# Performance work log

Hardware: AMD Instinct MI355X
Metric: run time of the kernel (lower is better)

## Reference

```python
import jax, jax.numpy as jnp
import numpy as np

D_MODEL = 1024
N_HEAD = 16
D_K = D_MODEL // N_HEAD
NEG = -1000000000.0


def setup_inputs() -> dict:
    key = jax.random.key(0)
    ks = jax.random.split(key, 12)
    B, S = 4, 2048
    scale = 1.0 / np.sqrt(D_MODEL)
    inp = {
        "q": jax.random.normal(ks[0], (B, S, D_MODEL), jnp.float32),
        "k": jax.random.normal(ks[1], (B, S, D_MODEL), jnp.float32),
        "v": jax.random.normal(ks[2], (B, S, D_MODEL), jnp.float32),
        "mask": jnp.ones((1, 1, S, S), jnp.int32),
        "w_Q": jax.random.normal(ks[3], (D_MODEL, D_MODEL), jnp.float32) * scale,
        "b_Q": jnp.zeros((D_MODEL,), jnp.float32),
        "w_K": jax.random.normal(ks[4], (D_MODEL, D_MODEL), jnp.float32) * scale,
        "b_K": jnp.zeros((D_MODEL,), jnp.float32),
        "w_V": jax.random.normal(ks[5], (D_MODEL, D_MODEL), jnp.float32) * scale,
        "b_V": jnp.zeros((D_MODEL,), jnp.float32),
        "w_O": jax.random.normal(ks[6], (D_MODEL, D_MODEL), jnp.float32) * scale,
        "b_O": jnp.zeros((D_MODEL,), jnp.float32),
    }
    return inp


def reference(q, k, v, mask, w_Q, b_Q, w_K, b_K, w_V, b_V, w_O, b_O):
    B, S, _ = q.shape
    # linear projections (torch Linear: x @ W^T + b)
    qp = q @ w_Q.T + b_Q
    kp = k @ w_K.T + b_K
    vp = v @ w_V.T + b_V
    # [B,S,D] -> [B,H,S,d_k]
    qh = qp.reshape(B, S, N_HEAD, D_K).transpose(0, 2, 1, 3)
    kh = kp.reshape(B, S, N_HEAD, D_K).transpose(0, 2, 1, 3)
    vh = vp.reshape(B, S, N_HEAD, D_K).transpose(0, 2, 1, 3)
    # scores [B,H,S,S]
    scores = jnp.einsum("bhqd,bhkd->bhqk", qh, kh) / jnp.sqrt(jnp.float32(D_K))
    scores = jnp.where(mask == 0, jnp.float32(NEG), scores)
    attn = jax.nn.softmax(scores, axis=-1)  # dropout p=0.0 -> identity
    ctx = jnp.einsum("bhqk,bhkd->bhqd", attn, vh)
    ctx = ctx.transpose(0, 2, 1, 3).reshape(B, S, D_MODEL)
    return ctx @ w_O.T + b_O
```

## Files before the change

kernel.cpp:

```cpp
#include <hip/hip_runtime.h>
#include <hip/hip_bf16.h>
#include <cmath>

#define D_MODEL 1024
#define N_HEAD 16
#define D_K 64

typedef __attribute__((ext_vector_type(8))) short short8;
typedef __attribute__((ext_vector_type(4))) float f32x4;
typedef __attribute__((ext_vector_type(16))) float f32x16;

#define GL_LDS16(gp, lp)                                                                   \
  __builtin_amdgcn_global_load_lds((const __attribute__((address_space(1))) unsigned int*)(gp), \
                                   (__attribute__((address_space(3))) unsigned int*)(lp), 16, 0, 0)

#if __has_builtin(__builtin_amdgcn_exp2f)
#define EXP2(x) __builtin_amdgcn_exp2f(x)
#else
#define EXP2(x) exp2f(x)
#endif

__device__ __forceinline__ unsigned short f2bu(float x) {
  __hip_bfloat16 h = __float2bfloat16(x);
  return *reinterpret_cast<unsigned short*>(&h);
}

__device__ __forceinline__ unsigned int cvtpk(float lo, float hi) {
  unsigned int r;
  asm("v_cvt_pk_bf16_f32 %0, %1, %2" : "=v"(r) : "v"(lo), "v"(hi));
  return r;
}

__device__ __forceinline__ float max3f(float a, float b, float c) {
  return fmaxf(fmaxf(a, b), c);
}

__device__ __forceinline__ void plswap(unsigned int& a, unsigned int& b) {
#if __has_builtin(__builtin_amdgcn_permlane32_swap)
  auto r = __builtin_amdgcn_permlane32_swap((int)a, (int)b, false, false);
  a = (unsigned int)r[0];
  b = (unsigned int)r[1];
#else
  unsigned int ax = (unsigned int)__shfl_xor((int)a, 32);
  unsigned int bx = (unsigned int)__shfl_xor((int)b, 32);
  bool hi = (threadIdx.x & 32) != 0;
  unsigned int na = hi ? bx : a;
  unsigned int nb = hi ? b : ax;
  a = na; b = nb;
#endif
}

__global__ __launch_bounds__(256) void f2b3_kernel(const float* __restrict__ a, const float* __restrict__ b,
                                                   const float* __restrict__ c,
                                                   unsigned short* __restrict__ oa, unsigned short* __restrict__ ob,
                                                   unsigned short* __restrict__ oc, int n) {
  const float* src = (blockIdx.y == 0) ? a : (blockIdx.y == 1) ? b : c;
  unsigned short* dst = (blockIdx.y == 0) ? oa : (blockIdx.y == 1) ? ob : oc;
  int i = (blockIdx.x * 256 + threadIdx.x) * 4;
  if (i >= n) return;
  float4 v = *reinterpret_cast<const float4*>(src + i);
  ushort4 o;
  o.x = f2bu(v.x); o.y = f2bu(v.y); o.z = f2bu(v.z); o.w = f2bu(v.w);
  *reinterpret_cast<ushort4*>(dst + i) = o;
}

__global__ __launch_bounds__(256) void f2b4_kernel(const float* __restrict__ a, const float* __restrict__ b,
                                                   const float* __restrict__ c, const float* __restrict__ d,
                                                   unsigned short* __restrict__ oa, unsigned short* __restrict__ ob,
                                                   unsigned short* __restrict__ oc, unsigned short* __restrict__ od,
                                                   int n) {
  const float* src = (blockIdx.y == 0) ? a : (blockIdx.y == 1) ? b : (blockIdx.y == 2) ? c : d;
  unsigned short* dst = (blockIdx.y == 0) ? oa : (blockIdx.y == 1) ? ob : (blockIdx.y == 2) ? oc : od;
  int i = (blockIdx.x * 256 + threadIdx.x) * 4;
  if (i >= n) return;
  float4 v = *reinterpret_cast<const float4*>(src + i);
  ushort4 o;
  o.x = f2bu(v.x); o.y = f2bu(v.y); o.z = f2bu(v.z); o.w = f2bu(v.w);
  *reinterpret_cast<ushort4*>(dst + i) = o;
}

template <int OUTF32>
__global__ __launch_bounds__(256) void gemm_bt_kernel(
    const unsigned short* __restrict__ A0, const unsigned short* __restrict__ A1,
    const unsigned short* __restrict__ A2,
    const unsigned short* __restrict__ W0, const unsigned short* __restrict__ W1,
    const unsigned short* __restrict__ W2,
    const float* __restrict__ b0, const float* __restrict__ b1, const float* __restrict__ b2,
    void* __restrict__ Cout, int Msub, int N, int K,
    float s0, float s1, float s2) {
  __shared__ __align__(16) unsigned short lA[3][128 * 32];
  __shared__ __align__(16) unsigned short lB[3][128 * 32];

  const int tid = threadIdx.x;
  const int lane = tid & 63;
  const int w = tid >> 6;
  const int wm = w >> 1, wn = w & 1;
  const int lr = lane & 15, lg = lane >> 4;
  const int wavebase = tid & ~63;

  int m0g, n0;
  {
    const int nbx = gridDim.x;
    const int nb = nbx * gridDim.y;
    int lin = blockIdx.y * nbx + blockIdx.x;
    int wid = lin;
    if ((nb & 7) == 0) wid = (lin & 7) * (nb >> 3) + (lin >> 3);
    n0 = (wid % nbx) * 128;
    m0g = (wid / nbx) * 128;
  }
  const int mtile = m0g >> 7;
  const int which = mtile / (Msub >> 7);
  const int m0 = m0g - which * Msub;
  const unsigned short* A  = (which == 0) ? A0 : (which == 1) ? A1 : A2;
  const unsigned short* Bw = (which == 0) ? W0 : (which == 1) ? W1 : W2;
  const float* bias = (which == 0) ? b0 : (which == 1) ? b1 : b2;
  const float oscale = (which == 0) ? s0 : (which == 1) ? s1 : s2;

  f32x4 acc[4][4] = {};

  const int swz = (lg ^ (lr & 3) ^ ((lr >> 2) & 3)) << 4;
  int avA[4], avB[4];
#pragma unroll
  for (int m = 0; m < 4; ++m) {
    avA[m] = (wm * 64 + m * 16 + lr) * 64 + swz;
    avB[m] = (wn * 64 + m * 16 + lr) * 64 + swz;
  }

  auto stage = [&](int buf, int k0) {
#pragma unroll
    for (int j = 0; j < 2; ++j) {
      int c = j * 256 + tid;
      int row = c >> 2, cc = c & 3;
      int gc = (cc ^ (row & 3) ^ ((row >> 2) & 3)) * 8;
      GL_LDS16(A + (size_t)(m0 + row) * K + k0 + gc,
               (char*)&lA[buf][0] + (j * 256 + wavebase) * 16);
    }
#pragma unroll
    for (int j = 0; j < 2; ++j) {
      int c = j * 256 + tid;
      int row = c >> 2, cc = c & 3;
      int gc = (cc ^ (row & 3) ^ ((row >> 2) & 3)) * 8;
      GL_LDS16(Bw + (size_t)(n0 + row) * K + k0 + gc,
               (char*)&lB[buf][0] + (j * 256 + wavebase) * 16);
    }
  };

  const int nk = K / 32;
  stage(0, 0);
  stage(1, 32);
  stage(2, 64);

  int buf = 0;
  for (int t = 0; t < nk; ++t) {
    if (t < nk - 2)       asm volatile("s_waitcnt vmcnt(8)" ::: "memory");
    else if (t == nk - 2) asm volatile("s_waitcnt vmcnt(4)" ::: "memory");
    else                  asm volatile("s_waitcnt vmcnt(0)" ::: "memory");
    __builtin_amdgcn_s_barrier();
    __builtin_amdgcn_sched_barrier(0);

    const char* pA = (const char*)&lA[buf][0];
    const char* pB = (const char*)&lB[buf][0];
    short8 a[4], bb[4];
#pragma unroll
    for (int m = 0; m < 4; ++m) a[m] = *reinterpret_cast<const short8*>(pA + avA[m]);
#pragma unroll
    for (int n = 0; n < 4; ++n) bb[n] = *reinterpret_cast<const short8*>(pB + avB[n]);

    __builtin_amdgcn_s_setprio(1);
#pragma unroll
    for (int m = 0; m < 4; ++m)
#pragma unroll
      for (int n = 0; n < 4; ++n)
        acc[m][n] = __builtin_amdgcn_mfma_f32_16x16x32_bf16(a[m], bb[n], acc[m][n], 0, 0, 0);
    __builtin_amdgcn_s_setprio(0);

    __builtin_amdgcn_s_barrier();
    __builtin_amdgcn_sched_barrier(0);
    if (t + 3 < nk) stage(buf, (t + 3) * 32);
    buf = (buf == 2) ? 0 : buf + 1;
  }

#pragma unroll
  for (int n = 0; n < 4; ++n) {
    const int gc = n0 + wn * 64 + n * 16 + lr;
    const float bn = bias[gc];
#pragma unroll
    for (int m = 0; m < 4; ++m) {
      const int gr0 = m0g + wm * 64 + m * 16 + lg * 4;
#pragma unroll
      for (int i = 0; i < 4; ++i) {
        float v = (acc[m][n][i] + bn) * oscale;
        if (OUTF32)
          reinterpret_cast<float*>(Cout)[(size_t)(gr0 + i) * N + gc] = v;
        else
          reinterpret_cast<unsigned short*>(Cout)[(size_t)(gr0 + i) * N + gc] = f2bu(v);
      }
    }
  }
}

__global__ __launch_bounds__(512, 4) void attn_kernel(
    const unsigned short* __restrict__ Qp, const unsigned short* __restrict__ Kp,
    const unsigned short* __restrict__ Vp, unsigned short* __restrict__ Ctx, int S) {
  __shared__ __align__(16) unsigned short Ks[2][64 * 64];
  __shared__ __align__(16) unsigned short Vt[2][64 * 64];

  const int tid = threadIdx.x;
  const int lane = tid & 63;
  const int wv = tid >> 6;
  const int l31 = lane & 31;
  const int hf = lane >> 5;

  const int nqb = gridDim.x;
  const int total = nqb * gridDim.y;
  int f = blockIdx.y * nqb + blockIdx.x;
  int g = ((total & 7) == 0) ? ((f & 7) * (total >> 3) + (f >> 3)) : f;
  const int bh = g / nqb;
  const int b = bh >> 4;
  const int head = bh & 15;
  const int q0 = (g % nqb) * 256;
  const int qrow = q0 + wv * 32 + l31;

  int av[4], av2[4];
#pragma unroll
  for (int c = 0; c < 4; ++c) {
    int chunk = ((c * 2 + hf) ^ (l31 & 7) ^ (l31 >> 3)) & 7;
    av[c] = l31 * 128 + (chunk << 4);
    av2[c] = (av[c] ^ 0x40) + 4096;
  }

  const unsigned short* qptr = Qp + (size_t)(b * S + qrow) * D_MODEL + head * 64;
  short8 qf[4];
#pragma unroll
  for (int ds = 0; ds < 4; ++ds)
    qf[ds] = *reinterpret_cast<const short8*>(qptr + ds * 16 + hf * 8);

  const int t256 = tid & 255;
  const int dblk = t256 & 15, kblk = t256 >> 4;
  const int dv0 = dblk * 4, key0 = kblk * 4;
  int wbyte[4];
#pragma unroll
  for (int j = 0; j < 4; ++j) {
    int row = dv0 + j;
    int slot = ((key0 >> 3) ^ (row & 7) ^ ((row >> 3) & 7)) & 7;
    wbyte[j] = row * 128 + (slot << 4) + ((key0 & 4) << 1);
  }

  float m_run = -1e30f, l_run = 0.0f;
  f32x16 oacc0 = {}, oacc1 = {};

  auto stageK = [&](int buf, int t) {
    const size_t baseK = (size_t)(b * S + t * 64) * D_MODEL + head * 64;
#pragma unroll
    for (int j = 0; j < 2; ++j) {
      int c = j * 256 + t256;
      int r = c >> 3, w8 = c & 7;
      int w8s = w8 ^ (r & 7) ^ ((r >> 3) & 7);
      GL_LDS16(Kp + baseK + (size_t)r * D_MODEL + w8s * 8,
               (char*)&Ks[buf][0] + (j * 256 + (t256 & ~63)) * 16);
    }
  };

  uint2 vr0, vr1, vr2, vr3;
  auto loadV = [&](int t) {
    const unsigned short* vptr =
        Vp + (size_t)(b * S + t * 64 + key0) * D_MODEL + head * 64 + dv0;
    vr0 = *reinterpret_cast<const uint2*>(vptr);
    vr1 = *reinterpret_cast<const uint2*>(vptr + D_MODEL);
    vr2 = *reinterpret_cast<const uint2*>(vptr + 2 * D_MODEL);
    vr3 = *reinterpret_cast<const uint2*>(vptr + 3 * D_MODEL);
  };

  if (wv >= 4) stageK(0, 0);
  else loadV(0);

  const int nt = S / 64;
  auto tile = [&](const int buf, const int t) {
    if (wv < 4) {
      char* vb = (char*)&Vt[buf][0];
      unsigned int o0x = __builtin_amdgcn_perm(vr1.x, vr0.x, 0x05040100u);
      unsigned int o0y = __builtin_amdgcn_perm(vr3.x, vr2.x, 0x05040100u);
      unsigned int o1x = __builtin_amdgcn_perm(vr1.x, vr0.x, 0x07060302u);
      unsigned int o1y = __builtin_amdgcn_perm(vr3.x, vr2.x, 0x07060302u);
      unsigned int o2x = __builtin_amdgcn_perm(vr1.y, vr0.y, 0x05040100u);
      unsigned int o2y = __builtin_amdgcn_perm(vr3.y, vr2.y, 0x05040100u);
      unsigned int o3x = __builtin_amdgcn_perm(vr1.y, vr0.y, 0x07060302u);
      unsigned int o3y = __builtin_amdgcn_perm(vr3.y, vr2.y, 0x07060302u);
      *reinterpret_cast<uint2*>(vb + wbyte[0]) = make_uint2(o0x, o0y);
      *reinterpret_cast<uint2*>(vb + wbyte[1]) = make_uint2(o1x, o1y);
      *reinterpret_cast<uint2*>(vb + wbyte[2]) = make_uint2(o2x, o2y);
      *reinterpret_cast<uint2*>(vb + wbyte[3]) = make_uint2(o3x, o3y);
    }
    __syncthreads();
    if (t + 1 < nt) {
      if (wv >= 4) stageK(buf ^ 1, t + 1);
      else loadV(t + 1);
    }

    const char* kbp = (const char*)&Ks[buf][0];
    const char* vbp = (const char*)&Vt[buf][0];

#pragma unroll
    for (int h2 = 0; h2 < 2; ++h2) {
      f32x16 sacc = {};
      __builtin_amdgcn_s_setprio(1);
#pragma unroll
      for (int ds = 0; ds < 4; ++ds) {
        short8 a0 = *reinterpret_cast<const short8*>(kbp + (h2 ? av2[ds] : av[ds]));
        sacc = __builtin_amdgcn_mfma_f32_32x32x16_bf16(a0, qf[ds], sacc, 0, 0, 0);
      }
      __builtin_amdgcn_s_setprio(0);

      float a0 = max3f(sacc[0], sacc[1], sacc[2]);
      float a1 = max3f(sacc[3], sacc[4], sacc[5]);
      float a2 = max3f(sacc[6], sacc[7], sacc[8]);
      float a3 = max3f(sacc[9], sacc[10], sacc[11]);
      float a4 = max3f(sacc[12], sacc[13], sacc[14]);
      float b0 = max3f(a0, a1, sacc[15]);
      float b1 = max3f(a2, a3, a4);
      float rmax_h = fmaxf(b0, b1);
      float rmax = fmaxf(rmax_h, __shfl_xor(rmax_h, 32));

      if (__any(rmax > m_run + 8.0f)) {
        float mnew = fmaxf(m_run, rmax);
        float al = EXP2(m_run - mnew);
        m_run = mnew;
        l_run *= al;
#pragma unroll
        for (int r = 0; r < 16; ++r) { oacc0[r] *= al; oacc1[r] *= al; }
      }

#pragma unroll
      for (int r = 0; r < 16; ++r) sacc[r] = EXP2(sacc[r] - m_run);

      float s0 = (sacc[0] + sacc[1]) + (sacc[2] + sacc[3]);
      float s1 = (sacc[4] + sacc[5]) + (sacc[6] + sacc[7]);
      float s2 = (sacc[8] + sacc[9]) + (sacc[10] + sacc[11]);
      float s3 = (sacc[12] + sacc[13]) + (sacc[14] + sacc[15]);
      float rsum = (s0 + s1) + (s2 + s3);
      rsum += __shfl_xor(rsum, 32);
      l_run += rsum;

      unsigned int W[8];
#pragma unroll
      for (int m = 0; m < 8; ++m) W[m] = cvtpk(sacc[2 * m], sacc[2 * m + 1]);
      short8 pf[2];
#pragma unroll
      for (int s = 0; s < 2; ++s) {
        unsigned int u0 = W[4 * s + 0], u2 = W[4 * s + 2];
        unsigned int u1 = W[4 * s + 1], u3 = W[4 * s + 3];
        plswap(u0, u2); plswap(u1, u3);
        int4 wvv = make_int4((int)u0, (int)u1, (int)u2, (int)u3);
        pf[s] = *reinterpret_cast<short8*>(&wvv);
      }

      __builtin_amdgcn_s_setprio(1);
#pragma unroll
      for (int s = 0; s < 2; ++s) {
        short8 va = *reinterpret_cast<const short8*>(vbp + av[h2 * 2 + s]);
        oacc0 = __builtin_amdgcn_mfma_f32_32x32x16_bf16(va, pf[s], oacc0, 0, 0, 0);
        short8 vb2 = *reinterpret_cast<const short8*>(vbp + av2[h2 * 2 + s]);
        oacc1 = __builtin_amdgcn_mfma_f32_32x32x16_bf16(vb2, pf[s], oacc1, 0, 0, 0);
      }
      __builtin_amdgcn_s_setprio(0);
    }
  };

  for (int t = 0; t < nt; t += 2) {
    tile(0, t);
    tile(1, t + 1);
  }

  const float linv = 1.0f / l_run;
  unsigned short* cp = Ctx + (size_t)(b * S + qrow) * D_MODEL + head * 64;
#pragma unroll
  for (int g2 = 0; g2 < 4; ++g2) {
    ushort4 o;
    o.x = f2bu(oacc0[4 * g2 + 0] * linv);
    o.y = f2bu(oacc0[4 * g2 + 1] * linv);
    o.z = f2bu(oacc0[4 * g2 + 2] * linv);
    o.w = f2bu(oacc0[4 * g2 + 3] * linv);
    *reinterpret_cast<ushort4*>(cp + 8 * g2 + 4 * hf) = o;
    ushort4 o2;
    o2.x = f2bu(oacc1[4 * g2 + 0] * linv);
    o2.y = f2bu(oacc1[4 * g2 + 1] * linv);
    o2.z = f2bu(oacc1[4 * g2 + 2] * linv);
    o2.w = f2bu(oacc1[4 * g2 + 3] * linv);
    *reinterpret_cast<ushort4*>(cp + 32 + 8 * g2 + 4 * hf) = o2;
  }
}

extern "C" void kernel_launch(void* const* d_in, const int* in_sizes, int n_in,
                              void* d_out, int out_size, void* d_ws, size_t ws_size,
                              hipStream_t stream) {
  const float* q  = (const float*)d_in[0];
  const float* k  = (const float*)d_in[1];
  const float* v  = (const float*)d_in[2];
  const float* wQ = (const float*)d_in[4];
  const float* bQ = (const float*)d_in[5];
  const float* wK = (const float*)d_in[6];
  const float* bK = (const float*)d_in[7];
  const float* wV = (const float*)d_in[8];
  const float* bV = (const float*)d_in[9];
  const float* wO = (const float*)d_in[10];
  const float* bO = (const float*)d_in[11];
  float* out = (float*)d_out;

  int S = 1;
  while ((long)S * S < (long)in_sizes[3]) S <<= 1;
  const int Bn = in_sizes[0] / (S * D_MODEL);
  const int M = Bn * S;

  unsigned short* xq   = (unsigned short*)d_ws;
  unsigned short* wqb  = xq + (size_t)M * D_MODEL;
  unsigned short* wkb  = wqb + (size_t)D_MODEL * D_MODEL;
  unsigned short* wvb  = wkb + (size_t)D_MODEL * D_MODEL;
  unsigned short* wob  = wvb + (size_t)D_MODEL * D_MODEL;
  unsigned short* qkvp = wob + (size_t)D_MODEL * D_MODEL;
  unsigned short* qp = qkvp;
  unsigned short* kp = qkvp + (size_t)M * D_MODEL;
  unsigned short* vp = qkvp + 2 * (size_t)M * D_MODEL;
  unsigned short* xk = (unsigned short*)d_out;
  unsigned short* xv = xk + (size_t)M * D_MODEL;

  const int DW = D_MODEL * D_MODEL;
  f2b4_kernel<<<dim3(DW / 1024, 4), 256, 0, stream>>>(wQ, wK, wV, wO, wqb, wkb, wvb, wob, DW);

  const int NX = M * D_MODEL;
  f2b3_kernel<<<dim3(NX / 1024, 3), 256, 0, stream>>>(q, k, v, xq, xk, xv, NX);

  const float qscale = 0.125f * 1.4426950408889634f;

  gemm_bt_kernel<0><<<dim3(D_MODEL / 128, 3 * M / 128), 256, 0, stream>>>(
      xq, xk, xv, wqb, wkb, wvb, bQ, bK, bV, qkvp, M, D_MODEL, D_MODEL,
      qscale, 1.0f, 1.0f);

  attn_kernel<<<dim3(S / 256, Bn * N_HEAD), 512, 0, stream>>>(qp, kp, vp, xq, S);

  gemm_bt_kernel<1><<<dim3(D_MODEL / 128, M / 128), 256, 0, stream>>>(
      xq, xq, xq, wob, wob, wob, bO, bO, bO, out, M, D_MODEL, D_MODEL,
      1.0f, 1.0f, 1.0f);
}
```

Baseline: 204.6 us.

## Use 256x256-tile GEMM with 8 waves for fused QKV projection

Adds a new bf16 MFMA GEMM kernel with 256x256 output tiles, 512 threads (8 waves, each computing 128x64), a triple-buffered LDS pipeline via global_load_lds, swizzled LDS layout, and grouped block ordering. It replaces the 128x128 GEMM for the QKV projection to raise arithmetic intensity per LDS/global byte. The larger tile needs 96KB of LDS and many accumulator registers, which limits occupancy, and the grid shrinks to 384 blocks, which may leave CUs unevenly loaded.

Result: slower. 229.7 us (+12.3%).

```diff
diff --git a/kernel.cpp b/kernel.cpp
--- a/kernel.cpp
+++ b/kernel.cpp
@@ -77,6 +77,119 @@
   ushort4 o;
   o.x = f2bu(v.x); o.y = f2bu(v.y); o.z = f2bu(v.z); o.w = f2bu(v.w);
   *reinterpret_cast<ushort4*>(dst + i) = o;
+}
+
+__global__ __launch_bounds__(512, 2) void gemm256_kernel(
+    const unsigned short* __restrict__ A0, const unsigned short* __restrict__ A1,
+    const unsigned short* __restrict__ A2,
+    const unsigned short* __restrict__ W0, const unsigned short* __restrict__ W1,
+    const unsigned short* __restrict__ W2,
+    const float* __restrict__ b0, const float* __restrict__ b1, const float* __restrict__ b2,
+    unsigned short* __restrict__ Cout, int Msub, int N, int K,
+    float s0, float s1, float s2) {
+  __shared__ __align__(16) unsigned short lA[3][256 * 32];
+  __shared__ __align__(16) unsigned short lB[3][256 * 32];
+
+  const int tid = threadIdx.x;
+  const int lane = tid & 63;
+  const int w = tid >> 6;
+  const int wm = w >> 2, wn = w & 3;
+  const int lr = lane & 15, lg = lane >> 4;
+  const int wavebase = tid & ~63;
+
+  int m0g, n0;
+  {
+    const int nbx = gridDim.x;
+    const int nb = nbx * gridDim.y;
+    int lin = blockIdx.y * nbx + blockIdx.x;
+    int wid = lin;
+    if ((nb & 7) == 0) wid = (lin & 7) * (nb >> 3) + (lin >> 3);
+    n0 = (wid % nbx) * 256;
+    m0g = (wid / nbx) * 256;
+  }
+  const int mtile = m0g >> 8;
+  const int which = mtile / (Msub >> 8);
+  const int m0 = m0g - which * Msub;
+  const unsigned short* A  = (which == 0) ? A0 : (which == 1) ? A1 : A2;
+  const unsigned short* Bw = (which == 0) ? W0 : (which == 1) ? W1 : W2;
+  const float* bias = (which == 0) ? b0 : (which == 1) ? b1 : b2;
+  const float oscale = (which == 0) ? s0 : (which == 1) ? s1 : s2;
+
+  f32x4 acc[8][4] = {};
+
+  const int swz = (lg ^ (lr & 3) ^ ((lr >> 2) & 3)) << 4;
+  int avA[8], avB[4];
+#pragma unroll
+  for (int m = 0; m < 8; ++m) avA[m] = (wm * 128 + m * 16 + lr) * 64 + swz;
+#pragma unroll
+  for (int n = 0; n < 4; ++n) avB[n] = (wn * 64 + n * 16 + lr) * 64 + swz;
+
+  auto stage = [&](int buf, int k0) {
+#pragma unroll
+    for (int j = 0; j < 2; ++j) {
+      int c = j * 512 + tid;
+      int row = c >> 2, cc = c & 3;
+      int gc = (cc ^ (row & 3) ^ ((row >> 2) & 3)) * 8;
+      GL_LDS16(A + (size_t)(m0 + row) * K + k0 + gc,
+               (char*)&lA[buf][0] + (j * 512 + wavebase) * 16);
+    }
+#pragma unroll
+    for (int j = 0; j < 2; ++j) {
+      int c = j * 512 + tid;
+      int row = c >> 2, cc = c & 3;
+      int gc = (cc ^ (row & 3) ^ ((row >> 2) & 3)) * 8;
+      GL_LDS16(Bw + (size_t)(n0 + row) * K + k0 + gc,
+               (char*)&lB[buf][0] + (j * 512 + wavebase) * 16);
+    }
+  };
+
+  const int nk = K / 32;
+  stage(0, 0);
+  stage(1, 32);
+  stage(2, 64);
+
+  int buf = 0;
+  for (int t = 0; t < nk; ++t) {
+    if (t < nk - 2)       asm volatile("s_waitcnt vmcnt(8)" ::: "memory");
+    else if (t == nk - 2) asm volatile("s_waitcnt vmcnt(4)" ::: "memory");
+    else                  asm volatile("s_waitcnt vmcnt(0)" ::: "memory");
+    __builtin_amdgcn_s_barrier();
+    __builtin_amdgcn_sched_barrier(0);
+
+    const char* pA = (const char*)&lA[buf][0];
+    const char* pB = (const char*)&lB[buf][0];
+    short8 a[8], bb[4];
+#pragma unroll
+    for (int m = 0; m < 8; ++m) a[m] = *reinterpret_cast<const short8*>(pA + avA[m]);
+#pragma unroll
+    for (int n = 0; n < 4; ++n) bb[n] = *reinterpret_cast<const short8*>(pB + avB[n]);
+
+    __builtin_amdgcn_s_setprio(1);
+#pragma unroll
+    for (int m = 0; m < 8; ++m)
+#pragma unroll
+      for (int n = 0; n < 4; ++n)
+        acc[m][n] = __builtin_amdgcn_mfma_f32_16x16x32_bf16(a[m], bb[n], acc[m][n], 0, 0, 0);
+    __builtin_amdgcn_s_setprio(0);
+
+    __builtin_amdgcn_s_barrier();
+    __builtin_amdgcn_sched_barrier(0);
+    if (t + 3 < nk) stage(buf, (t + 3) * 32);
+    buf = (buf == 2) ? 0 : buf + 1;
+  }
+
+#pragma unroll
+  for (int n = 0; n < 4; ++n) {
+    const int gc = n0 + wn * 64 + n * 16 + lr;
+    const float bn = bias[gc];
+#pragma unroll
+    for (int m = 0; m < 8; ++m) {
+      const int gr0 = m0g + wm * 128 + m * 16 + lg * 4;
+#pragma unroll
+      for (int i = 0; i < 4; ++i)
+        Cout[(size_t)(gr0 + i) * N + gc] = f2bu((acc[m][n][i] + bn) * oscale);
+    }
+  }
 }
 
 template <int OUTF32>
@@ -431,7 +544,7 @@
 
   const float qscale = 0.125f * 1.4426950408889634f;
 
-  gemm_bt_kernel<0><<<dim3(D_MODEL / 128, 3 * M / 128), 256, 0, stream>>>(
+  gemm256_kernel<<<dim3(D_MODEL / 256, 3 * M / 256), 512, 0, stream>>>(
       xq, xk, xv, wqb, wkb, wvb, bQ, bK, bV, qkvp, M, D_MODEL, D_MODEL,
       qscale, 1.0f, 1.0f);
 
```
